# Optimization experiments

Hardware: AMD Instinct MI355X
Metric: run time of the kernel (lower is better)

## Reference

```python
import jax, jax.numpy as jnp
import numpy as np


def setup_inputs() -> dict:
    key = jax.random.key(0)
    # [batch, heads, seq, head_dim]
    hidden_states = jax.random.normal(key, (2, 16, 2048, 64), dtype=jnp.float32)
    return {"hidden_states": hidden_states}


def reference(hidden_states):
    q = k = v = hidden_states
    # scores: [b, h, s, s] -- note: NO 1/sqrt(d) scaling, matching the original.
    scores = jnp.einsum("bhqd,bhkd->bhqk", q, k)
    a = jax.nn.softmax(scores, axis=-1)
    out = jnp.einsum("bhqk,bhkd->bhqd", a, v)
    return out
```

## Files before the change

kernel.cpp:

```cpp
#include <hip/hip_runtime.h>
#include <hip/hip_bf16.h>
#include <stdint.h>


typedef __bf16 bf16x8 __attribute__((ext_vector_type(8)));
typedef __bf16 bf16x2 __attribute__((ext_vector_type(2)));
typedef float f32x4 __attribute__((ext_vector_type(4)));
typedef float f32x16 __attribute__((ext_vector_type(16)));
typedef unsigned int u32x4v __attribute__((ext_vector_type(4)));

#define SEQ 2048
#define HD 64
#define KVB 64
#define NBH 32
#define NTILE (SEQ / KVB)
#define IMG_BYTES 8192
#define PAIR_BYTES 16384
#define WS_NEEDED ((size_t)NBH * NTILE * PAIR_BYTES)

#define QPB 128
#define RESCALE_THR 20.0f

__device__ __forceinline__ int swz(int row, int byteoff) {
    return byteoff ^ ((row & 7) << 4);
}

__device__ __forceinline__ float fexp2(float x) {
    float r;
    asm("v_exp_f32 %0, %1" : "=v"(r) : "v"(x));
    return r;
}

__device__ __forceinline__ unsigned pk_bf16(float a, float b) {
    bf16x2 v;
    v[0] = (__bf16)a;
    v[1] = (__bf16)b;
    return __builtin_bit_cast(unsigned, v);
}

#if __has_builtin(__builtin_amdgcn_global_load_lds)
#define HAVE_GLLDS 1
typedef const __attribute__((address_space(1))) unsigned int* gas_t;
typedef __attribute__((address_space(3))) unsigned int* las_t;
__device__ __forceinline__ void gl_lds16(const void* g, void* l) {
    __builtin_amdgcn_global_load_lds((gas_t)g, (las_t)l, 16, 0, 0);
}
#else
#define HAVE_GLLDS 0
#endif

__global__ __launch_bounds__(256)
void prep_kernel(const float* __restrict__ x, char* __restrict__ ws) {
    const int bh = blockIdx.y;
    const int tile = blockIdx.x;
    const int kv0 = tile * KVB;
    const int t = threadIdx.x;
    const int srow = t >> 2;
    const int scq = (t & 3) * 16;
    const float* __restrict__ X = x + (size_t)bh * SEQ * HD;
    char* __restrict__ img = ws + ((size_t)bh * NTILE + tile) * PAIR_BYTES;

    {
        const float* src = X + (size_t)(kv0 + srow) * HD + scq;
        float4 a = *(const float4*)(src);
        float4 b = *(const float4*)(src + 4);
        float4 c = *(const float4*)(src + 8);
        float4 d = *(const float4*)(src + 12);
        bf16x8 f0, f1;
        f0[0] = (__bf16)a.x; f0[1] = (__bf16)a.y; f0[2] = (__bf16)a.z; f0[3] = (__bf16)a.w;
        f0[4] = (__bf16)b.x; f0[5] = (__bf16)b.y; f0[6] = (__bf16)b.z; f0[7] = (__bf16)b.w;
        f1[0] = (__bf16)c.x; f1[1] = (__bf16)c.y; f1[2] = (__bf16)c.z; f1[3] = (__bf16)c.w;
        f1[4] = (__bf16)d.x; f1[5] = (__bf16)d.y; f1[6] = (__bf16)d.z; f1[7] = (__bf16)d.w;
        *(bf16x8*)&img[swz(srow, srow * 128 + scq * 2)] = f0;
        *(bf16x8*)&img[swz(srow, srow * 128 + scq * 2 + 16)] = f1;
    }
    {
        bf16x8 g0, g1;
#pragma unroll
        for (int j = 0; j < 8; ++j)
            g0[j] = (__bf16)X[(size_t)(kv0 + scq + j) * HD + srow];
#pragma unroll
        for (int j = 0; j < 8; ++j)
            g1[j] = (__bf16)X[(size_t)(kv0 + scq + 8 + j) * HD + srow];
        *(bf16x8*)&img[IMG_BYTES + swz(srow, srow * 128 + scq * 2)] = g0;
        *(bf16x8*)&img[IMG_BYTES + swz(srow, srow * 128 + scq * 2 + 16)] = g1;
    }
}

__global__ __launch_bounds__(256, 2)
void attn4_kernel(const float* __restrict__ x, const char* __restrict__ ws,
                  float* __restrict__ out) {
    __shared__ __align__(16) char kbuf[2][IMG_BYTES];
    __shared__ __align__(16) char vbuf[2][IMG_BYTES];

    const int wg = blockIdx.x;
    const int sid = (wg & 7) * 64 + (wg >> 3);
    const int bh = sid >> 4;
    const int q0 = (sid & 15) * QPB;

    const float* __restrict__ X = x + (size_t)bh * SEQ * HD;
    float* __restrict__ Op = out + (size_t)bh * SEQ * HD;
    const char* __restrict__ wsb = ws + (size_t)bh * NTILE * PAIR_BYTES;

    const int t = threadIdx.x;
    const int wave = t >> 6;
    const int lane = t & 63;
    const int ln = lane & 31;
    const int hi = lane >> 5;

    const int qbase = q0 + wave * 32;

    const float SCL = 1.4426950408889634f;
    bf16x8 qf[4];
    {
        const float* qsrc = X + (size_t)(qbase + ln) * HD;
#pragma unroll
        for (int dt = 0; dt < 4; ++dt) {
            const float* s8 = qsrc + dt * 16 + hi * 8;
            float4 a = *(const float4*)s8;
            float4 b = *(const float4*)(s8 + 4);
            bf16x8 f;
            f[0] = (__bf16)(a.x * SCL); f[1] = (__bf16)(a.y * SCL);
            f[2] = (__bf16)(a.z * SCL); f[3] = (__bf16)(a.w * SCL);
            f[4] = (__bf16)(b.x * SCL); f[5] = (__bf16)(b.y * SCL);
            f[6] = (__bf16)(b.z * SCL); f[7] = (__bf16)(b.w * SCL);
            qf[dt] = f;
        }
    }

    f32x16 acc0, acc1;
#pragma unroll
    for (int i = 0; i < 16; ++i) { acc0[i] = 0.f; acc1[i] = 0.f; }
    float m = -1e30f, l = 0.f;

#if HAVE_GLLDS
    {
        char* base = (wave & 2) ? &vbuf[0][(wave & 1) * 4096] : &kbuf[0][(wave & 1) * 4096];
        const char* sp = wsb + wave * 4096 + lane * 16;
#pragma unroll
        for (int j = 0; j < 4; ++j)
            gl_lds16(sp + j * 1024, base + j * 1024);
    }
#else
    {
        const char* img = wsb;
#pragma unroll
        for (int q = 0; q < 4; ++q) {
            bf16x8 d0 = *(const bf16x8*)(img + q * 4096 + t * 16);
            char* dst = (q & 2) ? &vbuf[0][(q & 1) * 4096] : &kbuf[0][(q & 1) * 4096];
            *(bf16x8*)&dst[t * 16] = d0;
        }
    }
#endif
    __syncthreads();

    for (int it = 0; it < NTILE; ++it) {
        const int cur = it & 1;

#if HAVE_GLLDS
        if (it + 1 < NTILE) {
            const char* img = wsb + (size_t)(it + 1) * PAIR_BYTES;
            char* base = (wave & 2) ? &vbuf[cur ^ 1][(wave & 1) * 4096]
                                    : &kbuf[cur ^ 1][(wave & 1) * 4096];
            const char* sp = img + wave * 4096 + lane * 16;
#pragma unroll
            for (int j = 0; j < 4; ++j)
                gl_lds16(sp + j * 1024, base + j * 1024);
        }
#else
        bf16x8 n0, n1, n2, n3;
        if (it + 1 < NTILE) {
            const char* img = wsb + (size_t)(it + 1) * PAIR_BYTES;
            n0 = *(const bf16x8*)(img + t * 16);
            n1 = *(const bf16x8*)(img + 4096 + t * 16);
            n2 = *(const bf16x8*)(img + 8192 + t * 16);
            n3 = *(const bf16x8*)(img + 12288 + t * 16);
        }
#endif

        const char* kb = kbuf[cur];
        const char* vb = vbuf[cur];

        f32x16 s0, s1;
#pragma unroll
        for (int i = 0; i < 16; ++i) { s0[i] = 0.f; s1[i] = 0.f; }
        __builtin_amdgcn_s_setprio(1);
#pragma unroll
        for (int dt = 0; dt < 4; ++dt) {
            const int r0 = ln;
            bf16x8 kf0 = *(const bf16x8*)&kb[swz(r0, r0 * 128 + dt * 32 + hi * 16)];
            s0 = __builtin_amdgcn_mfma_f32_32x32x16_bf16(kf0, qf[dt], s0, 0, 0, 0);
            const int r1 = 32 + ln;
            bf16x8 kf1 = *(const bf16x8*)&kb[swz(r1, r1 * 128 + dt * 32 + hi * 16)];
            s1 = __builtin_amdgcn_mfma_f32_32x32x16_bf16(kf1, qf[dt], s1, 0, 0, 0);
        }
        __builtin_amdgcn_s_setprio(0);

        float mx = s0[0];
#pragma unroll
        for (int i = 1; i < 16; ++i) mx = fmaxf(mx, s0[i]);
#pragma unroll
        for (int i = 0; i < 16; ++i) mx = fmaxf(mx, s1[i]);
        mx = fmaxf(mx, __shfl_xor(mx, 32));

        if (__any(mx > m + RESCALE_THR)) {
            const float mnew = fmaxf(m, mx);
            const float alpha = fexp2(m - mnew);
            l *= alpha;
            m = mnew;
#pragma unroll
            for (int r = 0; r < 16; ++r) {
                const int qr = (r & 3) + 8 * (r >> 2) + 4 * hi;
                const float ar = __shfl(alpha, qr);
                acc0[r] *= ar;
                acc1[r] *= ar;
            }
        }

        f32x16 e0, e1;
#pragma unroll
        for (int i = 0; i < 16; ++i) {
            e0[i] = fexp2(s0[i] - m);
            e1[i] = fexp2(s1[i] - m);
        }
        float ps = 0.f;
#pragma unroll
        for (int i = 0; i < 16; ++i) ps += e0[i] + e1[i];
        ps += __shfl_xor(ps, 32);
        l += ps;

        bf16x8 pa[4];
#pragma unroll
        for (int kt = 0; kt < 4; ++kt) {
            const f32x16& e = (kt & 2) ? e1 : e0;
            const int sx = 8 * (kt & 1);
            unsigned wA = pk_bf16(e[sx + 0], e[sx + 1]);
            unsigned wB = pk_bf16(e[sx + 2], e[sx + 3]);
            unsigned wC = pk_bf16(e[sx + 4], e[sx + 5]);
            unsigned wD = pk_bf16(e[sx + 6], e[sx + 7]);
            asm("v_permlane32_swap_b32 %0, %1" : "+v"(wA), "+v"(wC));
            asm("v_permlane32_swap_b32 %0, %1" : "+v"(wB), "+v"(wD));
            u32x4v w;
            w[0] = wA; w[1] = wB; w[2] = wC; w[3] = wD;
            pa[kt] = __builtin_bit_cast(bf16x8, w);
        }

        __builtin_amdgcn_s_setprio(1);
#pragma unroll
        for (int kt = 0; kt < 4; ++kt) {
            const int v0r = ln;
            bf16x8 vf0 = *(const bf16x8*)&vb[swz(v0r, v0r * 128 + kt * 32 + hi * 16)];
            acc0 = __builtin_amdgcn_mfma_f32_32x32x16_bf16(pa[kt], vf0, acc0, 0, 0, 0);
            const int v1r = 32 + ln;
            bf16x8 vf1 = *(const bf16x8*)&vb[swz(v1r, v1r * 128 + kt * 32 + hi * 16)];
            acc1 = __builtin_amdgcn_mfma_f32_32x32x16_bf16(pa[kt], vf1, acc1, 0, 0, 0);
        }
        __builtin_amdgcn_s_setprio(0);

#if !HAVE_GLLDS
        if (it + 1 < NTILE) {
            const int nxt = cur ^ 1;
            *(bf16x8*)&kbuf[nxt][t * 16] = n0;
            *(bf16x8*)&kbuf[nxt][4096 + t * 16] = n1;
            *(bf16x8*)&vbuf[nxt][t * 16] = n2;
            *(bf16x8*)&vbuf[nxt][4096 + t * 16] = n3;
        }
#endif
        __syncthreads();
    }

    const float invl = 1.f / l;
#pragma unroll
    for (int r = 0; r < 16; ++r) {
        const int qr = (r & 3) + 8 * (r >> 2) + 4 * hi;
        const float il = __shfl(invl, qr);
        float* dst = Op + (size_t)(qbase + qr) * HD + ln;
        dst[0]  = acc0[r] * il;
        dst[32] = acc1[r] * il;
    }
}

__global__ __launch_bounds__(256, 2)
void attn_fwd_kernel(const float* __restrict__ x, float* __restrict__ out) {
    __shared__ __align__(16) char k_lds[KVB * HD * 2];
    __shared__ __align__(16) char vt_lds[HD * KVB * 2];
    __shared__ __align__(16) char p_lds2[4][2][16 * KVB * 2];

    const int bh = blockIdx.y;
    const int q0 = blockIdx.x * 128;
    const float* __restrict__ X = x + (size_t)bh * SEQ * HD;
    float* __restrict__ Op = out + (size_t)bh * SEQ * HD;

    const int t = threadIdx.x;
    const int wave = t >> 6;
    const int lane = t & 63;
    const int lgrp = lane >> 4;
    const int lid = lane & 15;

    bf16x8 qf[2][2];
#pragma unroll
    for (int rt = 0; rt < 2; ++rt) {
        const int row = q0 + wave * 32 + rt * 16 + lid;
#pragma unroll
        for (int kc = 0; kc < 2; ++kc) {
            const float* src = X + (size_t)row * HD + kc * 32 + lgrp * 8;
            float4 a = *(const float4*)src;
            float4 b = *(const float4*)(src + 4);
            bf16x8 f;
            f[0] = (__bf16)a.x; f[1] = (__bf16)a.y; f[2] = (__bf16)a.z; f[3] = (__bf16)a.w;
            f[4] = (__bf16)b.x; f[5] = (__bf16)b.y; f[6] = (__bf16)b.z; f[7] = (__bf16)b.w;
            qf[rt][kc] = f;
        }
    }

    f32x4 acc[2][4];
    float m[2][4], l[2][4];
#pragma unroll
    for (int rt = 0; rt < 2; ++rt)
#pragma unroll
        for (int i = 0; i < 4; ++i) {
            acc[rt][i][0] = 0.f; acc[rt][i][1] = 0.f;
            acc[rt][i][2] = 0.f; acc[rt][i][3] = 0.f;
            m[rt][i] = -1e30f;
            l[rt][i] = 0.f;
        }

    const int srow = t >> 2;
    const int scq = (t & 3) * 16;

    for (int kv0 = 0; kv0 < SEQ; kv0 += KVB) {
        {
            const float* src = X + (size_t)(kv0 + srow) * HD + scq;
            float4 a = *(const float4*)(src);
            float4 b = *(const float4*)(src + 4);
            float4 c = *(const float4*)(src + 8);
            float4 d = *(const float4*)(src + 12);
            bf16x8 f0, f1;
            f0[0] = (__bf16)a.x; f0[1] = (__bf16)a.y; f0[2] = (__bf16)a.z; f0[3] = (__bf16)a.w;
            f0[4] = (__bf16)b.x; f0[5] = (__bf16)b.y; f0[6] = (__bf16)b.z; f0[7] = (__bf16)b.w;
            f1[0] = (__bf16)c.x; f1[1] = (__bf16)c.y; f1[2] = (__bf16)c.z; f1[3] = (__bf16)c.w;
            f1[4] = (__bf16)d.x; f1[5] = (__bf16)d.y; f1[6] = (__bf16)d.z; f1[7] = (__bf16)d.w;
            *(bf16x8*)&k_lds[swz(srow, srow * 128 + scq * 2)] = f0;
            *(bf16x8*)&k_lds[swz(srow, srow * 128 + scq * 2 + 16)] = f1;
        }
        {
            bf16x8 g0, g1;
#pragma unroll
            for (int j = 0; j < 8; ++j)
                g0[j] = (__bf16)X[(size_t)(kv0 + scq + j) * HD + srow];
#pragma unroll
            for (int j = 0; j < 8; ++j)
                g1[j] = (__bf16)X[(size_t)(kv0 + scq + 8 + j) * HD + srow];
            *(bf16x8*)&vt_lds[swz(srow, srow * 128 + scq * 2)] = g0;
            *(bf16x8*)&vt_lds[swz(srow, srow * 128 + scq * 2 + 16)] = g1;
        }
        __syncthreads();

#pragma unroll
        for (int rt = 0; rt < 2; ++rt) {
            f32x4 s[4];
#pragma unroll
            for (int kt = 0; kt < 4; ++kt) {
                f32x4 z = {0.f, 0.f, 0.f, 0.f};
#pragma unroll
                for (int kc = 0; kc < 2; ++kc) {
                    const int krow = kt * 16 + lid;
                    bf16x8 kfr = *(const bf16x8*)&k_lds[swz(krow, krow * 128 + (kc * 32 + lgrp * 8) * 2)];
                    z = __builtin_amdgcn_mfma_f32_16x16x32_bf16(qf[rt][kc], kfr, z, 0, 0, 0);
                }
                s[kt] = z;
            }

            char* pl = p_lds2[wave][rt];
#pragma unroll
            for (int r = 0; r < 4; ++r) {
                float mxv = fmaxf(fmaxf(s[0][r], s[1][r]), fmaxf(s[2][r], s[3][r]));
                mxv = fmaxf(mxv, __shfl_xor(mxv, 1));
                mxv = fmaxf(mxv, __shfl_xor(mxv, 2));
                mxv = fmaxf(mxv, __shfl_xor(mxv, 4));
                mxv = fmaxf(mxv, __shfl_xor(mxv, 8));
                const float mold = m[rt][r];
                const float mnew = fmaxf(mold, mxv);
                const float alpha = __expf(mold - mnew);
                const int prow = lgrp * 4 + r;
                float psum = 0.f;
#pragma unroll
                for (int kt = 0; kt < 4; ++kt) {
                    float p = __expf(s[kt][r] - mnew);
                    psum += p;
                    *(__bf16*)&pl[swz(prow, prow * 128 + (kt * 16 + lid) * 2)] = (__bf16)p;
                }
                psum += __shfl_xor(psum, 1);
                psum += __shfl_xor(psum, 2);
                psum += __shfl_xor(psum, 4);
                psum += __shfl_xor(psum, 8);
                l[rt][r] = l[rt][r] * alpha + psum;
                m[rt][r] = mnew;
#pragma unroll
                for (int ct = 0; ct < 4; ++ct)
                    acc[rt][ct][r] *= alpha;
            }

#pragma unroll
            for (int kc = 0; kc < 2; ++kc) {
                bf16x8 pfr = *(const bf16x8*)&pl[swz(lid, lid * 128 + (kc * 32 + lgrp * 8) * 2)];
#pragma unroll
                for (int ct = 0; ct < 4; ++ct) {
                    const int vrow = ct * 16 + lid;
                    bf16x8 vf = *(const bf16x8*)&vt_lds[swz(vrow, vrow * 128 + (kc * 32 + lgrp * 8) * 2)];
                    acc[rt][ct] = __builtin_amdgcn_mfma_f32_16x16x32_bf16(pfr, vf, acc[rt][ct], 0, 0, 0);
                }
            }
        }
        __syncthreads();
    }

#pragma unroll
    for (int rt = 0; rt < 2; ++rt)
#pragma unroll
        for (int r = 0; r < 4; ++r) {
            const float inv = 1.f / l[rt][r];
            const int row = q0 + wave * 32 + rt * 16 + lgrp * 4 + r;
            float* dst = Op + (size_t)row * HD + lid;
#pragma unroll
            for (int ct = 0; ct < 4; ++ct)
                dst[ct * 16] = acc[rt][ct][r] * inv;
        }
}

extern "C" void kernel_launch(void* const* d_in, const int* in_sizes, int n_in,
                              void* d_out, int out_size, void* d_ws, size_t ws_size,
                              hipStream_t stream) {
    const float* x = (const float*)d_in[0];
    float* out = (float*)d_out;
    if (ws_size >= WS_NEEDED) {
        char* ws = (char*)d_ws;
        dim3 pgrid(NTILE, NBH);
        hipLaunchKernelGGL(prep_kernel, pgrid, dim3(256), 0, stream, x, ws);
        hipLaunchKernelGGL(attn4_kernel, dim3((SEQ / QPB) * NBH), dim3(256), 0, stream,
                           x, ws, out);
    } else {
        dim3 grid(SEQ / 128, NBH);
        hipLaunchKernelGGL(attn_fwd_kernel, grid, dim3(256), 0, stream, x, out);
    }
}
```

Before: 70.06 us.

## Split KV range across two workgroups and merge partial softmax results

Each query tile now gets two workgroups, each covering half of the KV tiles. Each workgroup writes an unnormalized partial output plus its running max and sum to workspace, and a new merge kernel combines the two halves. The goal is to double the number of blocks and, with launch bounds raised to 4, the waves per CU, so latency hides better. In exchange this adds a third launch and extra global traffic for the fp32 partials. The LDS image layout also moves to an 8-byte-granular XOR swizzle read as two bf16x4 loads, which doubles the number of LDS read instructions.

Measured after the change: 77.20 us. 10.2% more time.

```diff
diff --git a/kernel.cpp b/kernel.cpp
--- a/kernel.cpp
+++ b/kernel.cpp
@@ -4,6 +4,7 @@
 
 
 typedef __bf16 bf16x8 __attribute__((ext_vector_type(8)));
+typedef __bf16 bf16x4 __attribute__((ext_vector_type(4)));
 typedef __bf16 bf16x2 __attribute__((ext_vector_type(2)));
 typedef float f32x4 __attribute__((ext_vector_type(4)));
 typedef float f32x16 __attribute__((ext_vector_type(16)));
@@ -16,7 +17,11 @@
 #define NTILE (SEQ / KVB)
 #define IMG_BYTES 8192
 #define PAIR_BYTES 16384
-#define WS_NEEDED ((size_t)NBH * NTILE * PAIR_BYTES)
+#define IMG_TOT ((size_t)NBH * NTILE * PAIR_BYTES)
+#define PART_BYTES ((size_t)2 * NBH * SEQ * HD * 4)
+#define ML_BYTES ((size_t)2 * NBH * SEQ * 8)
+#define WS_IMG IMG_TOT
+#define WS_SPLIT (IMG_TOT + PART_BYTES + ML_BYTES)
 
 #define QPB 128
 #define RESCALE_THR 20.0f
@@ -36,6 +41,17 @@
     v[0] = (__bf16)a;
     v[1] = (__bf16)b;
     return __builtin_bit_cast(unsigned, v);
+}
+
+__device__ __forceinline__ bf16x8 read_frag8(const char* base, int r, int p0) {
+    const char* rowp = base + r * 128;
+    const int rr = r & 15;
+    bf16x4 lo = *(const bf16x4*)(rowp + (((p0 + 0) ^ rr) << 3));
+    bf16x4 hi4 = *(const bf16x4*)(rowp + (((p0 + 1) ^ rr) << 3));
+    bf16x8 f;
+    f[0] = lo[0]; f[1] = lo[1]; f[2] = lo[2]; f[3] = lo[3];
+    f[4] = hi4[0]; f[5] = hi4[1]; f[6] = hi4[2]; f[7] = hi4[3];
+    return f;
 }
 
 #if __has_builtin(__builtin_amdgcn_global_load_lds)
@@ -60,36 +76,48 @@
     const float* __restrict__ X = x + (size_t)bh * SEQ * HD;
     char* __restrict__ img = ws + ((size_t)bh * NTILE + tile) * PAIR_BYTES;
 
+    const int rr = srow & 15;
+    const int p = scq >> 2;
+
     {
         const float* src = X + (size_t)(kv0 + srow) * HD + scq;
         float4 a = *(const float4*)(src);
         float4 b = *(const float4*)(src + 4);
         float4 c = *(const float4*)(src + 8);
         float4 d = *(const float4*)(src + 12);
-        bf16x8 f0, f1;
-        f0[0] = (__bf16)a.x; f0[1] = (__bf16)a.y; f0[2] = (__bf16)a.z; f0[3] = (__bf16)a.w;
-        f0[4] = (__bf16)b.x; f0[5] = (__bf16)b.y; f0[6] = (__bf16)b.z; f0[7] = (__bf16)b.w;
-        f1[0] = (__bf16)c.x; f1[1] = (__bf16)c.y; f1[2] = (__bf16)c.z; f1[3] = (__bf16)c.w;
-        f1[4] = (__bf16)d.x; f1[5] = (__bf16)d.y; f1[6] = (__bf16)d.z; f1[7] = (__bf16)d.w;
-        *(bf16x8*)&img[swz(srow, srow * 128 + scq * 2)] = f0;
-        *(bf16x8*)&img[swz(srow, srow * 128 + scq * 2 + 16)] = f1;
+        bf16x4 k0, k1, k2, k3;
+        k0[0] = (__bf16)a.x; k0[1] = (__bf16)a.y; k0[2] = (__bf16)a.z; k0[3] = (__bf16)a.w;
+        k1[0] = (__bf16)b.x; k1[1] = (__bf16)b.y; k1[2] = (__bf16)b.z; k1[3] = (__bf16)b.w;
+        k2[0] = (__bf16)c.x; k2[1] = (__bf16)c.y; k2[2] = (__bf16)c.z; k2[3] = (__bf16)c.w;
+        k3[0] = (__bf16)d.x; k3[1] = (__bf16)d.y; k3[2] = (__bf16)d.z; k3[3] = (__bf16)d.w;
+        char* rowp = img + srow * 128;
+        *(bf16x4*)(rowp + (((p + 0) ^ rr) << 3)) = k0;
+        *(bf16x4*)(rowp + (((p + 1) ^ rr) << 3)) = k1;
+        *(bf16x4*)(rowp + (((p + 2) ^ rr) << 3)) = k2;
+        *(bf16x4*)(rowp + (((p + 3) ^ rr) << 3)) = k3;
     }
     {
-        bf16x8 g0, g1;
-#pragma unroll
-        for (int j = 0; j < 8; ++j)
+        bf16x4 g0, g1, g2, g3;
+#pragma unroll
+        for (int j = 0; j < 4; ++j) {
             g0[j] = (__bf16)X[(size_t)(kv0 + scq + j) * HD + srow];
-#pragma unroll
-        for (int j = 0; j < 8; ++j)
-            g1[j] = (__bf16)X[(size_t)(kv0 + scq + 8 + j) * HD + srow];
-        *(bf16x8*)&img[IMG_BYTES + swz(srow, srow * 128 + scq * 2)] = g0;
-        *(bf16x8*)&img[IMG_BYTES + swz(srow, srow * 128 + scq * 2 + 16)] = g1;
-    }
-}
-
-__global__ __launch_bounds__(256, 2)
-void attn4_kernel(const float* __restrict__ x, const char* __restrict__ ws,
-                  float* __restrict__ out) {
+            g1[j] = (__bf16)X[(size_t)(kv0 + scq + 4 + j) * HD + srow];
+            g2[j] = (__bf16)X[(size_t)(kv0 + scq + 8 + j) * HD + srow];
+            g3[j] = (__bf16)X[(size_t)(kv0 + scq + 12 + j) * HD + srow];
+        }
+        char* rowp = img + IMG_BYTES + srow * 128;
+        *(bf16x4*)(rowp + (((p + 0) ^ rr) << 3)) = g0;
+        *(bf16x4*)(rowp + (((p + 1) ^ rr) << 3)) = g1;
+        *(bf16x4*)(rowp + (((p + 2) ^ rr) << 3)) = g2;
+        *(bf16x4*)(rowp + (((p + 3) ^ rr) << 3)) = g3;
+    }
+}
+
+template <int SPLIT>
+__global__ __launch_bounds__(256, 4)
+void attn_img_kernel(const float* __restrict__ x, const char* __restrict__ ws,
+                     float* __restrict__ outp, float* __restrict__ part,
+                     float2* __restrict__ ml) {
     __shared__ __align__(16) char kbuf[2][IMG_BYTES];
     __shared__ __align__(16) char vbuf[2][IMG_BYTES];
 
@@ -97,9 +125,11 @@
     const int sid = (wg & 7) * 64 + (wg >> 3);
     const int bh = sid >> 4;
     const int q0 = (sid & 15) * QPB;
+    const int half = SPLIT ? blockIdx.y : 0;
+    const int tile0 = SPLIT ? half * (NTILE / 2) : 0;
+    const int ntiles = SPLIT ? (NTILE / 2) : NTILE;
 
     const float* __restrict__ X = x + (size_t)bh * SEQ * HD;
-    float* __restrict__ Op = out + (size_t)bh * SEQ * HD;
     const char* __restrict__ wsb = ws + (size_t)bh * NTILE * PAIR_BYTES;
 
     const int t = threadIdx.x;
@@ -136,14 +166,14 @@
 #if HAVE_GLLDS
     {
         char* base = (wave & 2) ? &vbuf[0][(wave & 1) * 4096] : &kbuf[0][(wave & 1) * 4096];
-        const char* sp = wsb + wave * 4096 + lane * 16;
+        const char* sp = wsb + (size_t)tile0 * PAIR_BYTES + wave * 4096 + lane * 16;
 #pragma unroll
         for (int j = 0; j < 4; ++j)
             gl_lds16(sp + j * 1024, base + j * 1024);
     }
 #else
     {
-        const char* img = wsb;
+        const char* img = wsb + (size_t)tile0 * PAIR_BYTES;
 #pragma unroll
         for (int q = 0; q < 4; ++q) {
             bf16x8 d0 = *(const bf16x8*)(img + q * 4096 + t * 16);
@@ -154,12 +184,12 @@
 #endif
     __syncthreads();
 
-    for (int it = 0; it < NTILE; ++it) {
+    for (int it = 0; it < ntiles; ++it) {
         const int cur = it & 1;
 
 #if HAVE_GLLDS
-        if (it + 1 < NTILE) {
-            const char* img = wsb + (size_t)(it + 1) * PAIR_BYTES;
+        if (it + 1 < ntiles) {
+            const char* img = wsb + (size_t)(tile0 + it + 1) * PAIR_BYTES;
             char* base = (wave & 2) ? &vbuf[cur ^ 1][(wave & 1) * 4096]
                                     : &kbuf[cur ^ 1][(wave & 1) * 4096];
             const char* sp = img + wave * 4096 + lane * 16;
@@ -169,8 +199,8 @@
         }
 #else
         bf16x8 n0, n1, n2, n3;
-        if (it + 1 < NTILE) {
-            const char* img = wsb + (size_t)(it + 1) * PAIR_BYTES;
+        if (it + 1 < ntiles) {
+            const char* img = wsb + (size_t)(tile0 + it + 1) * PAIR_BYTES;
             n0 = *(const bf16x8*)(img + t * 16);
             n1 = *(const bf16x8*)(img + 4096 + t * 16);
             n2 = *(const bf16x8*)(img + 8192 + t * 16);
@@ -187,11 +217,10 @@
         __builtin_amdgcn_s_setprio(1);
 #pragma unroll
         for (int dt = 0; dt < 4; ++dt) {
-            const int r0 = ln;
-            bf16x8 kf0 = *(const bf16x8*)&kb[swz(r0, r0 * 128 + dt * 32 + hi * 16)];
+            const int p0 = dt * 4 + hi * 2;
+            bf16x8 kf0 = read_frag8(kb, ln, p0);
             s0 = __builtin_amdgcn_mfma_f32_32x32x16_bf16(kf0, qf[dt], s0, 0, 0, 0);
-            const int r1 = 32 + ln;
-            bf16x8 kf1 = *(const bf16x8*)&kb[swz(r1, r1 * 128 + dt * 32 + hi * 16)];
+            bf16x8 kf1 = read_frag8(kb, 32 + ln, p0);
             s1 = __builtin_amdgcn_mfma_f32_32x32x16_bf16(kf1, qf[dt], s1, 0, 0, 0);
         }
         __builtin_amdgcn_s_setprio(0);
@@ -248,17 +277,16 @@
         __builtin_amdgcn_s_setprio(1);
 #pragma unroll
         for (int kt = 0; kt < 4; ++kt) {
-            const int v0r = ln;
-            bf16x8 vf0 = *(const bf16x8*)&vb[swz(v0r, v0r * 128 + kt * 32 + hi * 16)];
+            const int p0 = kt * 4 + hi * 2;
+            bf16x8 vf0 = read_frag8(vb, ln, p0);
             acc0 = __builtin_amdgcn_mfma_f32_32x32x16_bf16(pa[kt], vf0, acc0, 0, 0, 0);
-            const int v1r = 32 + ln;
-            bf16x8 vf1 = *(const bf16x8*)&vb[swz(v1r, v1r * 128 + kt * 32 + hi * 16)];
+            bf16x8 vf1 = read_frag8(vb, 32 + ln, p0);
             acc1 = __builtin_amdgcn_mfma_f32_32x32x16_bf16(pa[kt], vf1, acc1, 0, 0, 0);
         }
         __builtin_amdgcn_s_setprio(0);
 
 #if !HAVE_GLLDS
-        if (it + 1 < NTILE) {
+        if (it + 1 < ntiles) {
             const int nxt = cur ^ 1;
             *(bf16x8*)&kbuf[nxt][t * 16] = n0;
             *(bf16x8*)&kbuf[nxt][4096 + t * 16] = n1;
@@ -269,15 +297,55 @@
         __syncthreads();
     }
 
-    const float invl = 1.f / l;
-#pragma unroll
-    for (int r = 0; r < 16; ++r) {
-        const int qr = (r & 3) + 8 * (r >> 2) + 4 * hi;
-        const float il = __shfl(invl, qr);
-        float* dst = Op + (size_t)(qbase + qr) * HD + ln;
-        dst[0]  = acc0[r] * il;
-        dst[32] = acc1[r] * il;
-    }
+    if (SPLIT) {
+        float* OP = part + ((size_t)(half * NBH + bh) * SEQ) * HD;
+#pragma unroll
+        for (int r = 0; r < 16; ++r) {
+            const int qr = (r & 3) + 8 * (r >> 2) + 4 * hi;
+            float* dst = OP + (size_t)(qbase + qr) * HD + ln;
+            dst[0]  = acc0[r];
+            dst[32] = acc1[r];
+        }
+        if (lane < 32)
+            ml[(size_t)(half * NBH + bh) * SEQ + qbase + lane] = make_float2(m, l);
+    } else {
+        float* Op = outp + (size_t)bh * SEQ * HD;
+        const float invl = 1.f / l;
+#pragma unroll
+        for (int r = 0; r < 16; ++r) {
+            const int qr = (r & 3) + 8 * (r >> 2) + 4 * hi;
+            const float il = __shfl(invl, qr);
+            float* dst = Op + (size_t)(qbase + qr) * HD + ln;
+            dst[0]  = acc0[r] * il;
+            dst[32] = acc1[r] * il;
+        }
+    }
+}
+
+__global__ __launch_bounds__(256)
+void merge_kernel(const float* __restrict__ part, const float2* __restrict__ ml,
+                  float* __restrict__ outp) {
+    const int t = threadIdx.x;
+    const size_t row = (size_t)blockIdx.x * 16 + (t >> 4);
+    const int c4 = t & 15;
+    const size_t NR = (size_t)NBH * SEQ;
+
+    const float2 a = ml[row];
+    const float2 b = ml[NR + row];
+    const float mN = fmaxf(a.x, b.x);
+    const float aA = fexp2(a.x - mN);
+    const float aB = fexp2(b.x - mN);
+    const float inv = 1.f / (a.y * aA + b.y * aB);
+
+    const f32x4* pA = (const f32x4*)part + row * 16 + c4;
+    const f32x4* pB = (const f32x4*)part + (NR + row) * 16 + c4;
+    f32x4 va = *pA;
+    f32x4 vb = *pB;
+    f32x4 o;
+#pragma unroll
+    for (int j = 0; j < 4; ++j)
+        o[j] = (va[j] * aA + vb[j] * aB) * inv;
+    *((f32x4*)outp + row * 16 + c4) = o;
 }
 
 __global__ __launch_bounds__(256, 2)
@@ -433,12 +501,21 @@
                               hipStream_t stream) {
     const float* x = (const float*)d_in[0];
     float* out = (float*)d_out;
-    if (ws_size >= WS_NEEDED) {
-        char* ws = (char*)d_ws;
+    char* ws = (char*)d_ws;
+    if (ws_size >= WS_SPLIT) {
+        float* part = (float*)(ws + IMG_TOT);
+        float2* ml = (float2*)(ws + IMG_TOT + PART_BYTES);
         dim3 pgrid(NTILE, NBH);
         hipLaunchKernelGGL(prep_kernel, pgrid, dim3(256), 0, stream, x, ws);
-        hipLaunchKernelGGL(attn4_kernel, dim3((SEQ / QPB) * NBH), dim3(256), 0, stream,
-                           x, ws, out);
+        hipLaunchKernelGGL((attn_img_kernel<1>), dim3(512, 2), dim3(256), 0, stream,
+                           x, ws, out, part, ml);
+        hipLaunchKernelGGL(merge_kernel, dim3(NBH * SEQ / 16), dim3(256), 0, stream,
+                           part, ml, out);
+    } else if (ws_size >= WS_IMG) {
+        dim3 pgrid(NTILE, NBH);
+        hipLaunchKernelGGL(prep_kernel, pgrid, dim3(256), 0, stream, x, ws);
+        hipLaunchKernelGGL((attn_img_kernel<0>), dim3(512, 1), dim3(256), 0, stream,
+                           x, ws, out, nullptr, nullptr);
     } else {
         dim3 grid(SEQ / 128, NBH);
         hipLaunchKernelGGL(attn_fwd_kernel, grid, dim3(256), 0, stream, x, out);
```
